# Kernel tuning notes

Hardware: AMD Instinct MI355X
Metric: run time of the kernel (lower is better)

The kernel has to match this reference:

```python
import jax, jax.numpy as jnp
import numpy as np

N = 10000        # total nodes in batch
E = 320000       # total edges (before self-loops)
D_IN = 128       # node_dim
H_DIM = 64       # hidden_dim
HEADS = 4
B = 64           # number of graphs
NUM_EDGES = 1024 # actor output dim


def _lin(k, i, o):
    return jax.random.normal(k, (i, o), jnp.float32) / np.sqrt(i)


def setup_inputs() -> dict:
    key = jax.random.key(0)
    ks = jax.random.split(key, 32)
    x = jax.random.normal(ks[0], (N, D_IN), jnp.float32)
    edge_index = jax.random.randint(ks[1], (2, E), 0, N, dtype=jnp.int64)
    batch = jnp.sort(jax.random.randint(ks[2], (N,), 0, B, dtype=jnp.int64))
    inp = dict(x=x, edge_index=edge_index, batch=batch)
    # GAT layer 1: in=D_IN, heads=4, out=H_DIM, concat
    inp['W1'] = _lin(ks[3], D_IN, HEADS * H_DIM)
    inp['as1'] = jax.random.normal(ks[4], (HEADS, H_DIM), jnp.float32) * 0.1
    inp['ad1'] = jax.random.normal(ks[5], (HEADS, H_DIM), jnp.float32) * 0.1
    inp['b1'] = jnp.zeros((HEADS * H_DIM,), jnp.float32)
    # GAT layer 2: in=4*H_DIM, heads=4, out=H_DIM, concat
    inp['W2'] = _lin(ks[6], HEADS * H_DIM, HEADS * H_DIM)
    inp['as2'] = jax.random.normal(ks[7], (HEADS, H_DIM), jnp.float32) * 0.1
    inp['ad2'] = jax.random.normal(ks[8], (HEADS, H_DIM), jnp.float32) * 0.1
    inp['b2'] = jnp.zeros((HEADS * H_DIM,), jnp.float32)
    # GAT layer 3: in=4*H_DIM, heads=1, out=H_DIM, mean (concat=False)
    inp['W3'] = _lin(ks[9], HEADS * H_DIM, H_DIM)
    inp['as3'] = jax.random.normal(ks[10], (1, H_DIM), jnp.float32) * 0.1
    inp['ad3'] = jax.random.normal(ks[11], (1, H_DIM), jnp.float32) * 0.1
    inp['b3'] = jnp.zeros((H_DIM,), jnp.float32)
    # actor MLP
    inp['Wa1'] = _lin(ks[12], H_DIM, H_DIM); inp['ba1'] = jnp.zeros((H_DIM,), jnp.float32)
    inp['Wa2'] = _lin(ks[13], H_DIM, NUM_EDGES); inp['ba2'] = jnp.zeros((NUM_EDGES,), jnp.float32)
    # critic MLP
    inp['Wc1'] = _lin(ks[14], H_DIM, H_DIM); inp['bc1'] = jnp.zeros((H_DIM,), jnp.float32)
    inp['Wc2'] = _lin(ks[15], H_DIM, 1); inp['bc2'] = jnp.zeros((1,), jnp.float32)
    return inp


def gat_layer(x, src, dst, W, a_src, a_dst, bias, heads, out_dim, concat):
    # PyG GATConv: linear -> edge attention -> per-dst softmax -> scatter-add
    n = x.shape[0]
    h = (x @ W).reshape(n, heads, out_dim)            # [N,H,D]
    s = (h * a_src).sum(-1)                           # [N,H] attention src term
    d = (h * a_dst).sum(-1)                           # [N,H]
    e = jax.nn.leaky_relu(s[src] + d[dst], 0.2)       # [Eall,H]
    m = jax.ops.segment_max(e, dst, num_segments=n)   # stable softmax per dst node
    w = jnp.exp(e - m[dst])
    alpha = w / jax.ops.segment_sum(w, dst, num_segments=n)[dst]
    agg = jax.ops.segment_sum(h[src] * alpha[..., None], dst, num_segments=n)  # [N,H,D]
    o = agg.reshape(n, heads * out_dim) if concat else agg.mean(axis=1)
    return o + bias


def forward(x, edge_index, batch, W1, as1, ad1, b1, W2, as2, ad2, b2,
            W3, as3, ad3, b3, Wa1, ba1, Wa2, ba2, Wc1, bc1, Wc2, bc2):
    n = x.shape[0]
    loop = jnp.arange(n, dtype=edge_index.dtype)
    src = jnp.concatenate([edge_index[0], loop])      # add_self_loops=True (PyG default)
    dst = jnp.concatenate([edge_index[1], loop])
    h = jax.nn.relu(gat_layer(x, src, dst, W1, as1, ad1, b1, HEADS, H_DIM, True))
    h = jax.nn.relu(gat_layer(h, src, dst, W2, as2, ad2, b2, HEADS, H_DIM, True))
    h = jax.nn.relu(gat_layer(h, src, dst, W3, as3, ad3, b3, 1, H_DIM, False))
    # global_mean_pool
    counts = jax.ops.segment_sum(jnp.ones((n,), h.dtype), batch, num_segments=B)
    pooled = jax.ops.segment_sum(h, batch, num_segments=B) / jnp.maximum(counts, 1.0)[:, None]
    # heads (dropout is identity at inference)
    action = jnp.tanh(jax.nn.relu(pooled @ Wa1 + ba1) @ Wa2 + ba2)
    value = jax.nn.relu(pooled @ Wc1 + bc1) @ Wc2 + bc2
    return action, value


def reference(x, edge_index, batch, W1, as1, ad1, b1, W2, as2, ad2, b2,
              W3, as3, ad3, b3, Wa1, ba1, Wa2, ba2, Wc1, bc1, Wc2, bc2):
    return forward(x, edge_index, batch, W1, as1, ad1, b1, W2, as2, ad2, b2,
                   W3, as3, ad3, b3, Wa1, ba1, Wa2, ba2, Wc1, bc1, Wc2, bc2)
```

## Files before the change

kernel.cpp:

```cpp
#include <hip/hip_runtime.h>
#include <hip/hip_bf16.h>

#define NN 10000
#define EE 320000
#define EALL (EE + NN)
#define BG 64
#define AOUT 1024

#define WTOT 191361
#define NX (NN * 128)
#define XV (NX / 8)
#define NSF 262144
#define NSI 131072

#define DRANGE 640
#define DNB 16
#define NSEG 64
#define ESEG 5157

typedef __hip_bfloat16 bf16;
typedef __attribute__((ext_vector_type(8))) short bf16x8;
typedef __attribute__((ext_vector_type(4))) float f32x4;

__device__ __forceinline__ unsigned short f2bf(float f) {
    bf16 h = __float2bfloat16(f);
    return *reinterpret_cast<unsigned short*>(&h);
}
__device__ __forceinline__ float bf2f(unsigned short u) {
    bf16 h;
    *reinterpret_cast<unsigned short*>(&h) = u;
    return __bfloat162float(h);
}
__device__ __forceinline__ int f_isfp32(const int* flags) {
    return (flags[2] > 0 || flags[3] > 50000) ? 1 : 0;
}

__global__ void k_detect(const unsigned short* __restrict__ x, const unsigned int* __restrict__ ei,
                         int* __restrict__ flags) {
    int i = blockIdx.x * 256 + threadIdx.x;
    bool nanp = false, zp = false, odd = false;
    if (i < NSF) {
        unsigned short h = x[i];
        nanp = (h & 0x7F80u) == 0x7F80u;
        zp = ((i & 1) == 0) && (h == 0);
    } else if (i < NSF + NSI) {
        int j = i - NSF;
        odd = ei[2 * j + 1] != 0u;
    }
    unsigned long long bn = __ballot(nanp);
    unsigned long long bz = __ballot(zp);
    unsigned long long bo = __ballot(odd);
    if ((threadIdx.x & 63) == 0) {
        if (bn) atomicAdd(&flags[2], __popcll(bn));
        if (bz) atomicAdd(&flags[3], __popcll(bz));
        if (bo) atomicOr(&flags[1], 1);
    }
}

struct WPtrs { const void* p[20]; };
__global__ void k_cvt_all(WPtrs wp, const void* __restrict__ xsrc,
                          const void* __restrict__ eisrc, const void* __restrict__ bsrc,
                          float* __restrict__ wf, int* __restrict__ ei32, int* __restrict__ b32,
                          unsigned short* __restrict__ x16,
                          unsigned short* __restrict__ w1t, unsigned short* __restrict__ w2t,
                          unsigned short* __restrict__ w3t,
                          const int* __restrict__ flags, int ffh, int fih) {
    const int sz[20] = {32768,256,256,256,65536,256,256,256,16384,64,64,64,4096,64,65536,1024,4096,64,64,1};
    int i = blockIdx.x * 256 + threadIdx.x;
    const int ff = (ffh >= 0) ? ffh : f_isfp32(flags);
    const int fi = (fih >= 0) ? fih : flags[1];
    if (i < WTOT) {
        int seg = 0, off = 0;
        while (i - off >= sz[seg]) { off += sz[seg]; seg++; }
        const void* src = wp.p[seg];
        int k = i - off;
        wf[i] = ff ? ((const float*)src)[k] : __bfloat162float(((const bf16*)src)[k]);
        return;
    }
    i -= WTOT;
    if (i < EE) {
        int j = i * 2;
        if (fi) {
            int2 v = ((const int2*)eisrc)[i];
            ei32[j] = v.x; ei32[j + 1] = v.y;
        } else {
            const long long* e8 = (const long long*)eisrc;
            ei32[j] = (int)e8[j]; ei32[j + 1] = (int)e8[j + 1];
        }
        return;
    }
    i -= EE;
    if (i < NN) { b32[i] = fi ? ((const int*)bsrc)[i] : (int)((const long long*)bsrc)[i]; return; }
    i -= NN;
    if (i < XV) {
        int k = i * 8;
        if (ff) {
            const float4* xs = (const float4*)((const float*)xsrc + k);
            float4 a = xs[0], b = xs[1];
            union { unsigned short u16[8]; uint4 v; } pk;
            pk.u16[0] = f2bf(a.x); pk.u16[1] = f2bf(a.y);
            pk.u16[2] = f2bf(a.z); pk.u16[3] = f2bf(a.w);
            pk.u16[4] = f2bf(b.x); pk.u16[5] = f2bf(b.y);
            pk.u16[6] = f2bf(b.z); pk.u16[7] = f2bf(b.w);
            *(uint4*)&x16[k] = pk.v;
        } else {
            *(uint4*)&x16[k] = ((const uint4*)xsrc)[i];
        }
        return;
    }
    i -= XV;
    if (i < 32768) {
        int k = i >> 8, c = i & 255;
        float v = ff ? ((const float*)wp.p[0])[i] : __bfloat162float(((const bf16*)wp.p[0])[i]);
        w1t[c * 128 + k] = f2bf(v);
        return;
    }
    i -= 32768;
    if (i < 65536) {
        int k = i >> 8, c = i & 255;
        float v = ff ? ((const float*)wp.p[4])[i] : __bfloat162float(((const bf16*)wp.p[4])[i]);
        w2t[c * 256 + k] = f2bf(v);
        return;
    }
    i -= 65536;
    if (i < 16384) {
        int k = i >> 6, c = i & 63;
        float v = ff ? ((const float*)wp.p[8])[i] : __bfloat162float(((const bf16*)wp.p[8])[i]);
        w3t[c * 256 + k] = f2bf(v);
    }
}
#define CVT_TOT (WTOT + EE + NN + XV + 32768 + 65536 + 16384)

__global__ __launch_bounds__(256) void k_fuse1(const int* __restrict__ ei, int* __restrict__ partial,
                                               const unsigned short* __restrict__ A16,
                                               const unsigned short* __restrict__ WT16,
                                               const float* __restrict__ asf,
                                               const float* __restrict__ adf,
                                               unsigned short* __restrict__ C16,
                                               float* __restrict__ sb, float* __restrict__ db) {
    __shared__ int bins[DRANGE];
    constexpr int LDW = 40;
    __shared__ unsigned short As[64 * LDW];
    __shared__ unsigned short Bs[64 * LDW];
    const int t = threadIdx.x;
    if (blockIdx.x < DNB * NSEG) {
        const int r0 = (blockIdx.x >> 6) * DRANGE;
        const int sg = blockIdx.x & 63;
        for (int i = t; i < DRANGE; i += 256) bins[i] = 0;
        __syncthreads();
        const int e1 = min(sg * ESEG + ESEG, EALL);
        for (int e = sg * ESEG + t; e < e1; e += 256) {
            int dst = (e < EE) ? ei[EE + e] : (e - EE);
            unsigned rel = dst - r0;
            if (rel < DRANGE) atomicAdd(&bins[rel], 1);
        }
        __syncthreads();
        for (int i = t; i < DRANGE; i += 256)
            partial[blockIdx.x * DRANGE + i] = bins[i];
        return;
    }
    constexpr int K = 128, M = 256, H = M / 64;
    const int u = blockIdx.x - DNB * NSEG;
    const int bx = u % 157;
    const int hh = u / 157;
    const int row0 = bx * 64;
    const int col0 = hh * 64;
    const int wv = t >> 6;
    const int lane = t & 63;
    const int m = lane & 15;
    const int q = lane >> 4;
    const int srow = t >> 2;
    const int skoff = (t & 3) * 8;

    f32x4 acc[4] = {};
    for (int k0 = 0; k0 < K; k0 += 32) {
        {
            int grow = row0 + srow;
            uint4 av = make_uint4(0u, 0u, 0u, 0u);
            if (grow < NN) av = *(const uint4*)&A16[(size_t)grow * K + k0 + skoff];
            *(uint4*)&As[srow * LDW + skoff] = av;
            uint4 bv = *(const uint4*)&WT16[(size_t)(col0 + srow) * K + k0 + skoff];
            *(uint4*)&Bs[srow * LDW + skoff] = bv;
        }
        __syncthreads();
        bf16x8 af = *(const bf16x8*)&As[(16 * wv + m) * LDW + q * 8];
#pragma unroll
        for (int ct = 0; ct < 4; ct++) {
            bf16x8 bfv = *(const bf16x8*)&Bs[(16 * ct + m) * LDW + q * 8];
            acc[ct] = __builtin_amdgcn_mfma_f32_16x16x32_bf16(af, bfv, acc[ct], 0, 0, 0);
        }
        __syncthreads();
    }
    float asv[4], adv[4];
#pragma unroll
    for (int ct = 0; ct < 4; ct++) {
        asv[ct] = asf[hh * 64 + 16 * ct + m];
        adv[ct] = adf[hh * 64 + 16 * ct + m];
    }
#pragma unroll
    for (int reg = 0; reg < 4; reg++) {
        int row = row0 + 16 * wv + q * 4 + reg;
        float ps = 0.f, pd = 0.f;
        if (row < NN) {
#pragma unroll
            for (int ct = 0; ct < 4; ct++) {
                float v = acc[ct][reg];
                C16[(size_t)row * M + col0 + 16 * ct + m] = f2bf(v);
                ps += v * asv[ct];
                pd += v * adv[ct];
            }
        }
#pragma unroll
        for (int off = 1; off < 16; off <<= 1) {
            ps += __shfl_xor(ps, off);
            pd += __shfl_xor(pd, off);
        }
        if (m == 0 && row < NN) { sb[row * H + hh] = ps; db[row * H + hh] = pd; }
    }
}

__global__ void k_seg(const int* __restrict__ partial, int* __restrict__ deg,
                      int* __restrict__ segpre) {
    int bin = blockIdx.x * 256 + threadIdx.x;
    if (bin >= NN) return;
    int r = bin / DRANGE, rel = bin - r * DRANGE;
    int s = 0;
    for (int sg = 0; sg < NSEG; sg++) {
        int idx = (r * NSEG + sg) * DRANGE + rel;
        int v = partial[idx];
        segpre[idx] = s;
        s += v;
    }
    deg[bin] = s;
}

__global__ void k_scan4(const int* __restrict__ deg, int* __restrict__ rowstart,
                        const int* __restrict__ batch, int* __restrict__ gstart) {
    __shared__ int part[1024];
    const int t = threadIdx.x;
    if (t <= BG) {
        int lo = 0, hi = NN;
        while (lo < hi) { int mid = (lo + hi) >> 1; if (batch[mid] < t) lo = mid + 1; else hi = mid; }
        gstart[t] = lo;
    }
    const int base = t * 10;
    int local[10];
    int s = 0;
    for (int i = 0; i < 10; i++) {
        int idx = base + i;
        int v = (idx < NN) ? deg[idx] : 0;
        local[i] = s; s += v;
    }
    part[t] = s; __syncthreads();
    for (int off = 1; off < 1024; off <<= 1) {
        int v = (t >= off) ? part[t - off] : 0;
        __syncthreads();
        part[t] += v;
        __syncthreads();
    }
    int pre = (t == 0) ? 0 : part[t - 1];
    for (int i = 0; i < 10; i++) {
        int idx = base + i;
        if (idx < NN) rowstart[idx] = pre + local[i];
    }
    if (t == 1023) rowstart[NN] = part[1023];
}

__global__ __launch_bounds__(256) void k_scatter3(const int* __restrict__ ei,
                                                  const int* __restrict__ rowstart,
                                                  const int* __restrict__ segpre,
                                                  int* __restrict__ ssrc) {
    __shared__ int cur[DRANGE];
    const int r0 = blockIdx.x * DRANGE;
    const int sg = blockIdx.y;
    for (int i = threadIdx.x; i < DRANGE; i += 256) {
        int bin = r0 + i;
        cur[i] = (bin < NN) ? rowstart[bin] + segpre[(blockIdx.x * NSEG + sg) * DRANGE + i] : 0;
    }
    __syncthreads();
    const int e1 = min(sg * ESEG + ESEG, EALL);
    for (int e = sg * ESEG + threadIdx.x; e < e1; e += 256) {
        int dst = (e < EE) ? ei[EE + e] : (e - EE);
        unsigned rel = dst - r0;
        if (rel < DRANGE) {
            int src = (e < EE) ? ei[e] : dst;
            int pos = atomicAdd(&cur[rel], 1);
            ssrc[pos] = src;
        }
    }
}

template<int K, int M>
__global__ __launch_bounds__(256) void k_gemm(const unsigned short* __restrict__ A16,
                                              const unsigned short* __restrict__ WT16,
                                              const float* __restrict__ asf,
                                              const float* __restrict__ adf,
                                              unsigned short* __restrict__ C16,
                                              float* __restrict__ sb, float* __restrict__ db) {
    constexpr int BK = 32;
    constexpr int H = M / 64;
    constexpr int LDW = 40;
    __shared__ unsigned short As[64 * LDW];
    __shared__ unsigned short Bs[64 * LDW];
    const int row0 = blockIdx.x * 64;
    const int col0 = blockIdx.y * 64;
    const int hh = blockIdx.y;
    const int t = threadIdx.x;
    const int wv = t >> 6;
    const int lane = t & 63;
    const int m = lane & 15;
    const int q = lane >> 4;
    const int srow = t >> 2;
    const int skoff = (t & 3) * 8;

    f32x4 acc[4] = {};

    for (int k0 = 0; k0 < K; k0 += BK) {
        {
            int grow = row0 + srow;
            uint4 av = make_uint4(0u, 0u, 0u, 0u);
            if (grow < NN) av = *(const uint4*)&A16[(size_t)grow * K + k0 + skoff];
            *(uint4*)&As[srow * LDW + skoff] = av;
            uint4 bv = *(const uint4*)&WT16[(size_t)(col0 + srow) * K + k0 + skoff];
            *(uint4*)&Bs[srow * LDW + skoff] = bv;
        }
        __syncthreads();
        bf16x8 af = *(const bf16x8*)&As[(16 * wv + m) * LDW + q * 8];
#pragma unroll
        for (int ct = 0; ct < 4; ct++) {
            bf16x8 bfv = *(const bf16x8*)&Bs[(16 * ct + m) * LDW + q * 8];
            acc[ct] = __builtin_amdgcn_mfma_f32_16x16x32_bf16(af, bfv, acc[ct], 0, 0, 0);
        }
        __syncthreads();
    }

    float asv[4], adv[4];
#pragma unroll
    for (int ct = 0; ct < 4; ct++) {
        asv[ct] = asf[hh * 64 + 16 * ct + m];
        adv[ct] = adf[hh * 64 + 16 * ct + m];
    }
#pragma unroll
    for (int reg = 0; reg < 4; reg++) {
        int row = row0 + 16 * wv + q * 4 + reg;
        float ps = 0.f, pd = 0.f;
        if (row < NN) {
#pragma unroll
            for (int ct = 0; ct < 4; ct++) {
                float v = acc[ct][reg];
                C16[(size_t)row * M + col0 + 16 * ct + m] = f2bf(v);
                ps += v * asv[ct];
                pd += v * adv[ct];
            }
        }
#pragma unroll
        for (int off = 1; off < 16; off <<= 1) {
            ps += __shfl_xor(ps, off);
            pd += __shfl_xor(pd, off);
        }
        if (m == 0 && row < NN) { sb[row * H + hh] = ps; db[row * H + hh] = pd; }
    }
}

template<int H>
__global__ void k_agg(const unsigned short* __restrict__ hbuf16, const float* __restrict__ sb,
                      const float* __restrict__ db, const int* __restrict__ rowstart,
                      const int* __restrict__ ssrc, const float* __restrict__ bias,
                      unsigned short* __restrict__ out16) {
    constexpr int M = H * 64;
    constexpr int LH = (H == 4) ? 2 : 0;
    constexpr int NW = M / 64;
    constexpr int CG = M / 8;
    constexpr int LCG = (H == 4) ? 5 : 3;
    const int n = blockIdx.x;
    const int tid = threadIdx.x;
    const int start = rowstart[n], end = rowstart[n + 1];
    const int slot = tid >> LH;
    const int hh = tid & (H - 1);
    const int wv = tid >> 6;
    const int lane = tid & 63;
    const int cg = tid & (CG - 1);
    const int eg = tid >> LCG;
    const int chh = (H == 4) ? (cg >> 3) : 0;
    __shared__ float wl[64 * H];
    __shared__ int srcl[64];
    __shared__ float accbuf[8 * M];
    __shared__ float smw[NW][H];
    __shared__ float sww[NW][H];
    const float dn = db[n * H + hh];

    float mymax = -3e38f;
    for (int p = start + slot; p < end; p += 64) {
        float e = sb[ssrc[p] * H + hh] + dn;
        e = e > 0.f ? e : 0.2f * e;
        mymax = fmaxf(mymax, e);
    }
#pragma unroll
    for (int off = H; off < 64; off <<= 1) mymax = fmaxf(mymax, __shfl_xor(mymax, off));
    float mh;
    if constexpr (NW > 1) {
        if (lane < H) smw[wv][lane] = mymax;
        __syncthreads();
        mh = smw[0][hh];
#pragma unroll
        for (int w = 1; w < NW; w++) mh = fmaxf(mh, smw[w][hh]);
    } else {
        mh = mymax;
    }

    float wsum = 0.f;
    float acc[8] = {};
    for (int c = start; c < end; c += 64) {
        const int cn = min(64, end - c);
        __syncthreads();
        if (slot < cn) {
            int s = ssrc[c + slot];
            float e = sb[s * H + hh] + dn;
            e = e > 0.f ? e : 0.2f * e;
            float wv2 = __expf(e - mh);
            wl[slot * H + hh] = wv2;
            wsum += wv2;
            if (hh == 0) srcl[slot] = s;
        }
        __syncthreads();
#pragma unroll 2
        for (int j = eg; j < cn; j += 8) {
            float wv2 = wl[j * H + chh];
            const bf16x8 v = *(const bf16x8*)&hbuf16[(size_t)srcl[j] * M + cg * 8];
#pragma unroll
            for (int i = 0; i < 8; i++)
                acc[i] += wv2 * bf2f((unsigned short)v[i]);
        }
    }

    {
        float* ab = &accbuf[eg * M + cg * 8];
#pragma unroll
        for (int i = 0; i < 8; i++) ab[i] = acc[i];
    }
#pragma unroll
    for (int off = H; off < 64; off <<= 1) wsum += __shfl_xor(wsum, off);
    if constexpr (NW > 1) { if (lane < H) sww[wv][lane] = wsum; }
    __syncthreads();

    float wsh;
    const int h2 = (H == 4) ? (tid >> 6) : 0;
    if constexpr (NW > 1) {
        wsh = sww[0][h2];
#pragma unroll
        for (int w = 1; w < NW; w++) wsh += sww[w][h2];
    } else {
        wsh = wsum;
    }

    float o = 0.f;
#pragma unroll
    for (int e8 = 0; e8 < 8; e8++) o += accbuf[e8 * M + tid];
    o = o / wsh + bias[tid];
    out16[(size_t)n * M + tid] = f2bf(fmaxf(o, 0.f));
}

__global__ __launch_bounds__(256) void k_final(const unsigned short* __restrict__ feat16,
                                               const int* __restrict__ gstart,
                                               const float* __restrict__ Wa1, const float* __restrict__ ba1,
                                               const float* __restrict__ Wc1, const float* __restrict__ bc1,
                                               const float* __restrict__ Wa2, const float* __restrict__ ba2,
                                               const float* __restrict__ Wc2, const float* __restrict__ bc2,
                                               float* __restrict__ out) {
    __shared__ float red[256];
    __shared__ float p[64];
    __shared__ float a[64], cc[64];
    const int g = blockIdx.x, t = threadIdx.x;
    const int d = t & 63, c = t >> 6;
    const int s = gstart[g], e = gstart[g + 1];
    float acc = 0.f;
    for (int n = s + c; n < e; n += 4) acc += bf2f(feat16[(size_t)n * 64 + d]);
    red[t] = acc; __syncthreads();
    if (c == 0) p[d] = (red[d] + red[64 + d] + red[128 + d] + red[192 + d])
                       / fmaxf((float)(e - s), 1.f);
    __syncthreads();
    if (t < 128) {
        int j = t & 63;
        const float* W  = (t < 64) ? Wa1 : Wc1;
        const float* bb = (t < 64) ? ba1 : bc1;
        float h = 0.f;
#pragma unroll 8
        for (int k = 0; k < 64; k++) h += p[k] * W[k * 64 + j];
        h = fmaxf(h + bb[j], 0.f);
        if (t < 64) a[j] = h; else cc[j] = h;
    }
    __syncthreads();
    float o[4] = {0.f, 0.f, 0.f, 0.f};
    for (int k = 0; k < 64; k++) {
        float ak = a[k];
#pragma unroll
        for (int q = 0; q < 4; q++) o[q] += ak * Wa2[k * AOUT + t + 256 * q];
    }
#pragma unroll
    for (int q = 0; q < 4; q++)
        out[g * AOUT + t + 256 * q] = tanhf(o[q] + ba2[t + 256 * q]);
    if (t == 0) {
        float v = 0.f;
        for (int k = 0; k < 64; k++) v += cc[k] * Wc2[k];
        out[BG * AOUT + g] = v + bc2[0];
    }
}

extern "C" void kernel_launch(void* const* d_in, const int* in_sizes, int n_in,
                              void* d_out, int out_size, void* d_ws, size_t ws_size,
                              hipStream_t stream) {
    float* out = (float*)d_out;

    char* w = (char*)d_ws;
    auto alloc = [&](size_t bytes) { void* p = (void*)w; w += (bytes + 255) & ~size_t(255); return p; };
    float* wf      = (float*)alloc((size_t)WTOT * 4);
    int*   ei32    = (int*)alloc((size_t)2 * EE * 4);
    int*   b32     = (int*)alloc((size_t)NN * 4);
    unsigned short* x16    = (unsigned short*)alloc((size_t)NX * 2);
    unsigned short* w1t    = (unsigned short*)alloc((size_t)32768 * 2);
    unsigned short* w2t    = (unsigned short*)alloc((size_t)65536 * 2);
    unsigned short* w3t    = (unsigned short*)alloc((size_t)16384 * 2);
    unsigned short* actA16 = (unsigned short*)alloc((size_t)NN * 256 * 2);
    unsigned short* actB16 = (unsigned short*)alloc((size_t)NN * 256 * 2);
    float* sb      = (float*)alloc((size_t)NN * 4 * 4);
    float* db      = (float*)alloc((size_t)NN * 4 * 4);
    int*   partial = (int*)alloc((size_t)DNB * NSEG * DRANGE * 4);
    int*   segpre  = (int*)alloc((size_t)DNB * NSEG * DRANGE * 4);
    int*   deg     = (int*)alloc((size_t)NN * 4);
    int*   flags   = (int*)alloc(64);
    int*   rowstart= (int*)alloc((size_t)(NN + 1) * 4);
    int*   ssrc    = (int*)alloc((size_t)EALL * 4);
    int*   gstart  = (int*)alloc((size_t)(BG + 1) * 4);

    int ffh = -1, fih = -1;
    if (in_sizes && n_in >= 2) {
        long long xs = in_sizes[0];
        if (xs == (long long)NX * 4) ffh = 1;
        else if (xs == (long long)NX * 2) ffh = 0;
        long long es = in_sizes[1];
        if (es == (long long)2 * EE * 8) fih = 0;
        else if (es == (long long)2 * EE * 4) fih = 1;
    }
    if (ffh < 0 || fih < 0) {
        hipMemsetAsync(flags, 0, 64, stream);
        k_detect<<<(NSF + NSI + 255) / 256, 256, 0, stream>>>(
            (const unsigned short*)d_in[0], (const unsigned int*)d_in[1], flags);
    }

    WPtrs wp;
    for (int s = 0; s < 20; s++) wp.p[s] = d_in[3 + s];
    k_cvt_all<<<(CVT_TOT + 255) / 256, 256, 0, stream>>>(
        wp, d_in[0], d_in[1], d_in[2], wf, ei32, b32, x16, w1t, w2t, w3t, flags, ffh, fih);

    const int wsz[20] = {32768,256,256,256,65536,256,256,256,16384,64,64,64,4096,64,65536,1024,4096,64,64,1};
    int woff[20]; int acc = 0;
    for (int s = 0; s < 20; s++) { woff[s] = acc; acc += wsz[s]; }
    const float *as1f = wf + woff[1], *ad1f = wf + woff[2], *b1f = wf + woff[3];
    const float *as2f = wf + woff[5], *ad2f = wf + woff[6], *b2f = wf + woff[7];
    const float *as3f = wf + woff[9], *ad3f = wf + woff[10], *b3f = wf + woff[11];
    const float *Wa1f = wf + woff[12], *ba1f = wf + woff[13], *Wa2f = wf + woff[14], *ba2f = wf + woff[15];
    const float *Wc1f = wf + woff[16], *bc1f = wf + woff[17], *Wc2f = wf + woff[18], *bc2f = wf + woff[19];

    k_fuse1<<<DNB * NSEG + 628, 256, 0, stream>>>(ei32, partial,
                                                  x16, w1t, as1f, ad1f, actA16, sb, db);

    k_seg<<<(NN + 255) / 256, 256, 0, stream>>>(partial, deg, segpre);
    k_scan4<<<1, 1024, 0, stream>>>(deg, rowstart, b32, gstart);
    k_scatter3<<<dim3(DNB, NSEG), 256, 0, stream>>>(ei32, rowstart, segpre, ssrc);

    k_agg<4><<<NN, 256, 0, stream>>>(actA16, sb, db, rowstart, ssrc, b1f, actB16);

    k_gemm<256, 256><<<dim3(157, 4), 256, 0, stream>>>(actB16, w2t, as2f, ad2f, actA16, sb, db);
    k_agg<4><<<NN, 256, 0, stream>>>(actA16, sb, db, rowstart, ssrc, b2f, actB16);

    k_gemm<256, 64><<<dim3(157, 1), 256, 0, stream>>>(actB16, w3t, as3f, ad3f, actA16, sb, db);
    k_agg<1><<<NN, 64, 0, stream>>>(actA16, sb, db, rowstart, ssrc, b3f, actB16);

    k_final<<<BG, 256, 0, stream>>>(actB16, gstart,
                                    Wa1f, ba1f, Wc1f, bc1f, Wa2f, ba2f, Wc2f, bc2f, out);
}
```

Measured before the change: 270.2 us.

## Fold dtype detection into conversion kernel and widen degree-histogram ranges

After: 240.6 us. 1.12x faster.

```diff
diff --git a/kernel.cpp b/kernel.cpp
--- a/kernel.cpp
+++ b/kernel.cpp
@@ -10,11 +10,9 @@
 #define WTOT 191361
 #define NX (NN * 128)
 #define XV (NX / 8)
-#define NSF 262144
-#define NSI 131072
-
-#define DRANGE 640
-#define DNB 16
+
+#define DRANGE 2560
+#define DNB 4
 #define NSEG 64
 #define ESEG 5157
 
@@ -31,44 +29,51 @@
     *reinterpret_cast<unsigned short*>(&h) = u;
     return __bfloat162float(h);
 }
-__device__ __forceinline__ int f_isfp32(const int* flags) {
-    return (flags[2] > 0 || flags[3] > 50000) ? 1 : 0;
-}
-
-__global__ void k_detect(const unsigned short* __restrict__ x, const unsigned int* __restrict__ ei,
-                         int* __restrict__ flags) {
-    int i = blockIdx.x * 256 + threadIdx.x;
-    bool nanp = false, zp = false, odd = false;
-    if (i < NSF) {
-        unsigned short h = x[i];
-        nanp = (h & 0x7F80u) == 0x7F80u;
-        zp = ((i & 1) == 0) && (h == 0);
-    } else if (i < NSF + NSI) {
-        int j = i - NSF;
-        odd = ei[2 * j + 1] != 0u;
-    }
-    unsigned long long bn = __ballot(nanp);
-    unsigned long long bz = __ballot(zp);
-    unsigned long long bo = __ballot(odd);
-    if ((threadIdx.x & 63) == 0) {
-        if (bn) atomicAdd(&flags[2], __popcll(bn));
-        if (bz) atomicAdd(&flags[3], __popcll(bz));
-        if (bo) atomicOr(&flags[1], 1);
-    }
-}
 
 struct WPtrs { const void* p[20]; };
-__global__ void k_cvt_all(WPtrs wp, const void* __restrict__ xsrc,
+__global__ __launch_bounds__(256) void k_cvt_all(WPtrs wp, const void* __restrict__ xsrc,
                           const void* __restrict__ eisrc, const void* __restrict__ bsrc,
                           float* __restrict__ wf, int* __restrict__ ei32, int* __restrict__ b32,
                           unsigned short* __restrict__ x16,
                           unsigned short* __restrict__ w1t, unsigned short* __restrict__ w2t,
                           unsigned short* __restrict__ w3t,
-                          const int* __restrict__ flags, int ffh, int fih) {
+                          int ffh, int fih) {
+    __shared__ int sff, sfi;
+    int ff, fi;
+    if (ffh >= 0 && fih >= 0) {
+        ff = ffh; fi = fih;
+    } else {
+        const int t = threadIdx.x;
+        bool nanp = false, odd = false;
+        {
+            const uint4* xs4 = (const uint4*)xsrc;
+            uint4 a = xs4[t * 8 + 0], b = xs4[t * 8 + 4];
+            const unsigned int wds[8] = {a.x, a.y, a.z, a.w, b.x, b.y, b.z, b.w};
+#pragma unroll
+            for (int k = 0; k < 8; k++) {
+                unsigned int w2 = wds[k];
+                if ((w2 & 0x7F80u) == 0x7F80u || ((w2 >> 16) & 0x7F80u) == 0x7F80u) nanp = true;
+            }
+        }
+        {
+            const unsigned int* eu = (const unsigned int*)eisrc;
+            odd = eu[2 * t + 1] != 0u;
+        }
+        unsigned long long bn = __ballot(nanp);
+        unsigned long long bo = __ballot(odd);
+        if (t == 0) { sff = 0; sfi = 0; }
+        __syncthreads();
+        if ((t & 63) == 0) {
+            if (bn) atomicOr(&sff, 1);
+            if (bo) atomicOr(&sfi, 1);
+        }
+        __syncthreads();
+        ff = (ffh >= 0) ? ffh : sff;
+        fi = (fih >= 0) ? fih : sfi;
+    }
+
     const int sz[20] = {32768,256,256,256,65536,256,256,256,16384,64,64,64,4096,64,65536,1024,4096,64,64,1};
     int i = blockIdx.x * 256 + threadIdx.x;
-    const int ff = (ffh >= 0) ? ffh : f_isfp32(flags);
-    const int fi = (fih >= 0) ? fih : flags[1];
     if (i < WTOT) {
         int seg = 0, off = 0;
         while (i - off >= sz[seg]) { off += sz[seg]; seg++; }
@@ -138,12 +143,11 @@
                                                const float* __restrict__ adf,
                                                unsigned short* __restrict__ C16,
                                                float* __restrict__ sb, float* __restrict__ db) {
-    __shared__ int bins[DRANGE];
     constexpr int LDW = 40;
-    __shared__ unsigned short As[64 * LDW];
-    __shared__ unsigned short Bs[64 * LDW];
+    __shared__ alignas(16) char smem[DRANGE * 4];
     const int t = threadIdx.x;
     if (blockIdx.x < DNB * NSEG) {
+        int* bins = (int*)smem;
         const int r0 = (blockIdx.x >> 6) * DRANGE;
         const int sg = blockIdx.x & 63;
         for (int i = t; i < DRANGE; i += 256) bins[i] = 0;
@@ -159,6 +163,8 @@
             partial[blockIdx.x * DRANGE + i] = bins[i];
         return;
     }
+    unsigned short* As = (unsigned short*)smem;
+    unsigned short* Bs = As + 64 * LDW;
     constexpr int K = 128, M = 256, H = M / 64;
     const int u = blockIdx.x - DNB * NSEG;
     const int bx = u % 157;
@@ -527,7 +533,6 @@
     int*   partial = (int*)alloc((size_t)DNB * NSEG * DRANGE * 4);
     int*   segpre  = (int*)alloc((size_t)DNB * NSEG * DRANGE * 4);
     int*   deg     = (int*)alloc((size_t)NN * 4);
-    int*   flags   = (int*)alloc(64);
     int*   rowstart= (int*)alloc((size_t)(NN + 1) * 4);
     int*   ssrc    = (int*)alloc((size_t)EALL * 4);
     int*   gstart  = (int*)alloc((size_t)(BG + 1) * 4);
@@ -541,16 +546,11 @@
         if (es == (long long)2 * EE * 8) fih = 0;
         else if (es == (long long)2 * EE * 4) fih = 1;
     }
-    if (ffh < 0 || fih < 0) {
-        hipMemsetAsync(flags, 0, 64, stream);
-        k_detect<<<(NSF + NSI + 255) / 256, 256, 0, stream>>>(
-            (const unsigned short*)d_in[0], (const unsigned int*)d_in[1], flags);
-    }
 
     WPtrs wp;
     for (int s = 0; s < 20; s++) wp.p[s] = d_in[3 + s];
     k_cvt_all<<<(CVT_TOT + 255) / 256, 256, 0, stream>>>(
-        wp, d_in[0], d_in[1], d_in[2], wf, ei32, b32, x16, w1t, w2t, w3t, flags, ffh, fih);
+        wp, d_in[0], d_in[1], d_in[2], wf, ei32, b32, x16, w1t, w2t, w3t, ffh, fih);
 
     const int wsz[20] = {32768,256,256,256,65536,256,256,256,16384,64,64,64,4096,64,65536,1024,4096,64,64,1};
     int woff[20]; int acc = 0;
```
